# Kernel tuning notes

Measured on AMD Instinct MI355X. Metric: run time of the kernel, lower is better.

Reference implementation:

```python
import jax, jax.numpy as jnp
import numpy as np

B, E, C = 32, 256, 7           # batch, max events, cards per event
D, NA, MP = 256, 8, 9          # d_model, n_actions, max_players
LN_EPS = 1e-5


def setup_inputs() -> dict:
    key = jax.random.key(0)
    ks = jax.random.split(key, 24)

    def tbl(k, shape):  # embedding-table init
        return jax.random.normal(k, shape, jnp.float32) * 0.02

    def lin(k, fan_in, fan_out):  # torch Linear-style init (W stored as (in, out))
        bound = 1.0 / np.sqrt(fan_in)
        k1, k2 = jax.random.split(k)
        W = jax.random.uniform(k1, (fan_in, fan_out), jnp.float32, -bound, bound)
        b = jax.random.uniform(k2, (fan_out,), jnp.float32, -bound, bound)
        return W, b

    W_scalar, b_scalar = lin(ks[10], 2, D)
    W_bet, b_bet = lin(ks[11], MP, D)
    W_action, b_action = lin(ks[12], NA, D)
    W_combine, b_combine = lin(ks[13], D * 7, D)

    return {
        "card_ids": jax.random.randint(ks[0], (B, E, C), 0, 53, jnp.int32),
        "hero_pos": jax.random.randint(ks[1], (B, E), 0, MP, jnp.int32),
        "acting_pos": jax.random.randint(ks[2], (B, E), 0, MP, jnp.int32),
        "num_players": jax.random.randint(ks[3], (B, E), 0, MP + 1, jnp.int32),
        "seq_lengths": jax.random.randint(ks[4], (B,), 1, E + 1, jnp.int32),
        "scalars": jax.random.uniform(ks[5], (B, E, 2), jnp.float32),
        "bets": jax.random.uniform(ks[6], (B, E, MP), jnp.float32),
        "action": jax.random.normal(ks[7], (B, E, NA), jnp.float32),
        "card_table": tbl(ks[14], (53, D)),
        "source_table": tbl(ks[15], (2, D)),
        "hero_table": tbl(ks[16], (MP, D)),
        "acting_table": tbl(ks[17], (MP, D)),
        "nump_table": tbl(ks[18], (MP + 1, D)),
        "W_scalar": W_scalar, "b_scalar": b_scalar,
        "W_bet": W_bet, "b_bet": b_bet,
        "W_action": W_action, "b_action": b_action,
        "W_combine": W_combine, "b_combine": b_combine,
        "ln_gamma": jnp.ones((D,), jnp.float32),
        "ln_beta": jnp.zeros((D,), jnp.float32),
    }


def reference(card_ids, hero_pos, acting_pos, num_players, seq_lengths,
              scalars, bets, action,
              card_table, source_table, hero_table, acting_table, nump_table,
              W_scalar, b_scalar, W_bet, b_bet, W_action, b_action,
              W_combine, b_combine, ln_gamma, ln_beta):
    # gathers
    card_embs = card_table[card_ids]                       # (B,E,7,D)
    source_ids = jnp.array([0, 0, 0, 0, 0, 1, 1], jnp.int32)
    source_embs = source_table[source_ids]                 # (7,D)
    hero_emb = hero_table[hero_pos]                        # (B,E,D)
    acting_emb = acting_table[acting_pos]                  # (B,E,D)
    nump_emb = nump_table[num_players]                     # (B,E,D)
    # small linears
    scalar_emb = scalars @ W_scalar + b_scalar             # (B,E,D)
    bet_emb = bets @ W_bet + b_bet                         # (B,E,D)
    action_emb = action @ W_action + b_action              # (B,E,D)
    # context shared across the 7 cards of an event
    context = jnp.concatenate(
        [hero_emb, acting_emb, nump_emb, scalar_emb, bet_emb, action_emb], axis=-1
    )                                                      # (B,E,6D)
    context = jnp.broadcast_to(context[:, :, None, :], (B, E, C, 6 * D))
    combined = jnp.concatenate([card_embs, context], axis=-1)  # (B,E,7,7D)
    h = combined @ W_combine + b_combine                   # (B,E,7,D)
    # LayerNorm
    mu = jnp.mean(h, axis=-1, keepdims=True)
    var = jnp.mean(jnp.square(h - mu), axis=-1, keepdims=True)
    h = (h - mu) * jax.lax.rsqrt(var + LN_EPS) * ln_gamma + ln_beta
    out = h + source_embs                                  # (B,E,7,D)
    # zero out padded events (original leaves padding as zeros)
    event_mask = (jnp.arange(E)[None, :] < seq_lengths[:, None]).astype(out.dtype)  # (B,E)
    out = out * event_mask[:, :, None, None]
    embeddings = out.reshape(B, E * C, D)
    mask = jnp.repeat(event_mask, C, axis=1)               # (B, E*7)
    return embeddings, mask
```

## Files before the change

kernel.cpp:

```cpp
#include <hip/hip_runtime.h>
#include <hip/hip_bf16.h>
#include <cstddef>

static constexpr int Bdim = 32;
static constexpr int Edim = 256;
static constexpr int Cdim = 7;
static constexpr int Ddim = 256;

__device__ float g_tabs[101 * Ddim];

__global__ __launch_bounds__(256) void precompute_tables(
    const float* __restrict__ card_table,
    const float* __restrict__ hero_table,
    const float* __restrict__ acting_table,
    const float* __restrict__ nump_table,
    const float* __restrict__ W_scalar, const float* __restrict__ b_scalar,
    const float* __restrict__ W_bet,    const float* __restrict__ b_bet,
    const float* __restrict__ W_action, const float* __restrict__ b_action,
    const float* __restrict__ W_combine, const float* __restrict__ b_combine)
{
    __shared__ float src[Ddim];
    const int r = blockIdx.x;
    const int d = threadIdx.x;
    float acc = 0.0f;

    if (r < 100) {
        const float* srcp;
        int off;
        if      (r < 53) { srcp = card_table   + (size_t)r        * Ddim; off = 0;    }
        else if (r < 62) { srcp = hero_table   + (size_t)(r - 53) * Ddim; off = 256;  }
        else if (r < 71) { srcp = acting_table + (size_t)(r - 62) * Ddim; off = 512;  }
        else if (r < 81) { srcp = nump_table   + (size_t)(r - 71) * Ddim; off = 768;  }
        else if (r < 83) { srcp = W_scalar     + (size_t)(r - 81) * Ddim; off = 1024; }
        else if (r < 92) { srcp = W_bet        + (size_t)(r - 83) * Ddim; off = 1280; }
        else             { srcp = W_action     + (size_t)(r - 92) * Ddim; off = 1536; }
        src[d] = srcp[d];
        __syncthreads();
        const float* w = W_combine + (size_t)off * Ddim + d;
        #pragma unroll 4
        for (int k = 0; k < Ddim; ++k)
            acc = fmaf(src[k], w[(size_t)k * Ddim], acc);
    } else {
        const int   offs[3] = {1024, 1280, 1536};
        const float* bias[3] = {b_scalar, b_bet, b_action};
        for (int t = 0; t < 3; ++t) {
            __syncthreads();
            src[d] = bias[t][d];
            __syncthreads();
            const float* w = W_combine + (size_t)offs[t] * Ddim + d;
            #pragma unroll 4
            for (int k = 0; k < Ddim; ++k)
                acc = fmaf(src[k], w[(size_t)k * Ddim], acc);
        }
        acc += b_combine[d];
    }
    g_tabs[(size_t)r * Ddim + d] = acc;
}

__device__ __forceinline__ float4 ld4(const float* p) {
    return *reinterpret_cast<const float4*>(p);
}
__device__ __forceinline__ void add4(float4& a, const float4 b) {
    a.x += b.x; a.y += b.y; a.z += b.z; a.w += b.w;
}
__device__ __forceinline__ void fma4(float4& a, const float s, const float4 b) {
    a.x = fmaf(s, b.x, a.x);
    a.y = fmaf(s, b.y, a.y);
    a.z = fmaf(s, b.z, a.z);
    a.w = fmaf(s, b.w, a.w);
}

__global__ __launch_bounds__(256) void event_embed(
    const int* __restrict__ card_ids,
    const int* __restrict__ hero_pos,
    const int* __restrict__ acting_pos,
    const int* __restrict__ num_players,
    const int* __restrict__ seq_lengths,
    const float* __restrict__ scalars,
    const float* __restrict__ bets,
    const float* __restrict__ action,
    const float* __restrict__ source_table,
    const float* __restrict__ ln_gamma,
    const float* __restrict__ ln_beta,
    float* __restrict__ out_emb,
    float* __restrict__ out_mask)
{
    const int wave = threadIdx.x >> 6;
    const int lane = threadIdx.x & 63;
    const int g = (blockIdx.x << 2) + wave;
    const int b = g >> 8;
    const int e = g & 255;
    const int d0 = lane << 2;

    const float* cardP = g_tabs;
    const float* heroP = cardP + 53 * Ddim;
    const float* actP  = heroP +  9 * Ddim;
    const float* numP  = actP  +  9 * Ddim;
    const float* WsP   = numP  + 10 * Ddim;
    const float* WbP   = WsP   +  2 * Ddim;
    const float* WaP   = WbP   +  9 * Ddim;
    const float* bP    = WaP   +  8 * Ddim;

    const float maskf = (e < seq_lengths[b]) ? 1.0f : 0.0f;

    float4 ctx = ld4(bP + d0);
    add4(ctx, ld4(heroP + (size_t)hero_pos[g]    * Ddim + d0));
    add4(ctx, ld4(actP  + (size_t)acting_pos[g]  * Ddim + d0));
    add4(ctx, ld4(numP  + (size_t)num_players[g] * Ddim + d0));
    fma4(ctx, scalars[(size_t)g * 2 + 0], ld4(WsP + d0));
    fma4(ctx, scalars[(size_t)g * 2 + 1], ld4(WsP + Ddim + d0));
    #pragma unroll
    for (int j = 0; j < 9; ++j)
        fma4(ctx, bets[(size_t)g * 9 + j], ld4(WbP + j * Ddim + d0));
    #pragma unroll
    for (int j = 0; j < 8; ++j)
        fma4(ctx, action[(size_t)g * 8 + j], ld4(WaP + j * Ddim + d0));

    const float4 gam = ld4(ln_gamma + d0);
    const float4 bta = ld4(ln_beta + d0);
    const float4 s0v = ld4(source_table + d0);
    const float4 s1v = ld4(source_table + Ddim + d0);

    #pragma unroll
    for (int c = 0; c < Cdim; ++c) {
        const int cid = card_ids[(size_t)g * Cdim + c];
        float4 h = ld4(cardP + (size_t)cid * Ddim + d0);
        add4(h, ctx);

        float s  = h.x + h.y + h.z + h.w;
        float sq = h.x * h.x + h.y * h.y + h.z * h.z + h.w * h.w;
        #pragma unroll
        for (int off = 32; off > 0; off >>= 1) {
            s  += __shfl_xor(s,  off, 64);
            sq += __shfl_xor(sq, off, 64);
        }
        const float mean = s * (1.0f / 256.0f);
        const float var  = fmaf(-mean, mean, sq * (1.0f / 256.0f));
        const float inv  = rsqrtf(var + 1e-5f);

        const float4 sv = (c < 5) ? s0v : s1v;
        float4 o;
        o.x = (fmaf((h.x - mean) * inv, gam.x, bta.x) + sv.x) * maskf;
        o.y = (fmaf((h.y - mean) * inv, gam.y, bta.y) + sv.y) * maskf;
        o.z = (fmaf((h.z - mean) * inv, gam.z, bta.z) + sv.z) * maskf;
        o.w = (fmaf((h.w - mean) * inv, gam.w, bta.w) + sv.w) * maskf;
        *reinterpret_cast<float4*>(out_emb + ((size_t)g * Cdim + c) * Ddim + d0) = o;
    }

    if (lane < Cdim)
        out_mask[(size_t)g * Cdim + lane] = maskf;
}

extern "C" void kernel_launch(void* const* d_in, const int* in_sizes, int n_in,
                              void* d_out, int out_size, void* d_ws, size_t ws_size,
                              hipStream_t stream)
{
    (void)in_sizes; (void)n_in; (void)d_ws; (void)ws_size; (void)out_size;

    const int*   card_ids    = (const int*)d_in[0];
    const int*   hero_pos    = (const int*)d_in[1];
    const int*   acting_pos  = (const int*)d_in[2];
    const int*   num_players = (const int*)d_in[3];
    const int*   seq_lengths = (const int*)d_in[4];
    const float* scalars     = (const float*)d_in[5];
    const float* bets        = (const float*)d_in[6];
    const float* action      = (const float*)d_in[7];
    const float* card_table  = (const float*)d_in[8];
    const float* source_tab  = (const float*)d_in[9];
    const float* hero_table  = (const float*)d_in[10];
    const float* acting_tab  = (const float*)d_in[11];
    const float* nump_table  = (const float*)d_in[12];
    const float* W_scalar    = (const float*)d_in[13];
    const float* b_scalar    = (const float*)d_in[14];
    const float* W_bet       = (const float*)d_in[15];
    const float* b_bet       = (const float*)d_in[16];
    const float* W_action    = (const float*)d_in[17];
    const float* b_action    = (const float*)d_in[18];
    const float* W_combine   = (const float*)d_in[19];
    const float* b_combine   = (const float*)d_in[20];
    const float* ln_gamma    = (const float*)d_in[21];
    const float* ln_beta     = (const float*)d_in[22];

    float* out_emb  = (float*)d_out;
    float* out_mask = out_emb + (size_t)Bdim * Edim * Cdim * Ddim;

    hipLaunchKernelGGL(precompute_tables, dim3(101), dim3(256), 0, stream,
                       card_table, hero_table, acting_tab, nump_table,
                       W_scalar, b_scalar, W_bet, b_bet, W_action, b_action,
                       W_combine, b_combine);

    const int nEvents = Bdim * Edim;
    hipLaunchKernelGGL(event_embed, dim3(nEvents / 4), dim3(256), 0, stream,
                       card_ids, hero_pos, acting_pos, num_players, seq_lengths,
                       scalars, bets, action, source_tab, ln_gamma, ln_beta,
                       out_emb, out_mask);
}
```

Before: 162.8 us.

## Split table precompute over K chunks and use nontemporal output stores

The table precompute GEMV, which ran on 101 blocks each looping over 256 K values, is split into 808 blocks that each cover a 32-wide K chunk. Partial sums go to workspace and a second small kernel reduces them and adds the combine bias. The main kernel's output writes become nontemporal stores to reduce cache pollution from the large streaming output. This adds one kernel launch and a workspace round-trip, and relies on d_ws being large enough.

```diff
diff --git a/kernel.cpp b/kernel.cpp
--- a/kernel.cpp
+++ b/kernel.cpp
@@ -9,7 +9,7 @@
 
 __device__ float g_tabs[101 * Ddim];
 
-__global__ __launch_bounds__(256) void precompute_tables(
+__global__ __launch_bounds__(256) void precompute_partial(
     const float* __restrict__ card_table,
     const float* __restrict__ hero_table,
     const float* __restrict__ acting_table,
@@ -17,11 +17,12 @@
     const float* __restrict__ W_scalar, const float* __restrict__ b_scalar,
     const float* __restrict__ W_bet,    const float* __restrict__ b_bet,
     const float* __restrict__ W_action, const float* __restrict__ b_action,
-    const float* __restrict__ W_combine, const float* __restrict__ b_combine)
-{
-    __shared__ float src[Ddim];
-    const int r = blockIdx.x;
-    const int d = threadIdx.x;
+    const float* __restrict__ W_combine,
+    float* __restrict__ partials)
+{
+    const int r  = blockIdx.x >> 3;
+    const int kc = blockIdx.x & 7;
+    const int d  = threadIdx.x;
     float acc = 0.0f;
 
     if (r < 100) {
@@ -34,27 +35,36 @@
         else if (r < 83) { srcp = W_scalar     + (size_t)(r - 81) * Ddim; off = 1024; }
         else if (r < 92) { srcp = W_bet        + (size_t)(r - 83) * Ddim; off = 1280; }
         else             { srcp = W_action     + (size_t)(r - 92) * Ddim; off = 1536; }
-        src[d] = srcp[d];
-        __syncthreads();
-        const float* w = W_combine + (size_t)off * Ddim + d;
-        #pragma unroll 4
-        for (int k = 0; k < Ddim; ++k)
-            acc = fmaf(src[k], w[(size_t)k * Ddim], acc);
+        const int k0 = kc << 5;
+        const float* w = W_combine + ((size_t)off + k0) * Ddim + d;
+        #pragma unroll
+        for (int k = 0; k < 32; ++k)
+            acc = fmaf(srcp[k0 + k], w[(size_t)k * Ddim], acc);
     } else {
-        const int   offs[3] = {1024, 1280, 1536};
-        const float* bias[3] = {b_scalar, b_bet, b_action};
-        for (int t = 0; t < 3; ++t) {
-            __syncthreads();
-            src[d] = bias[t][d];
-            __syncthreads();
-            const float* w = W_combine + (size_t)offs[t] * Ddim + d;
-            #pragma unroll 4
-            for (int k = 0; k < Ddim; ++k)
-                acc = fmaf(src[k], w[(size_t)k * Ddim], acc);
+        const int q0 = kc * 96;
+        #pragma unroll
+        for (int q = q0; q < q0 + 96; ++q) {
+            const float s = (q < 256) ? b_scalar[q]
+                          : (q < 512) ? b_bet[q - 256]
+                                      : b_action[q - 512];
+            acc = fmaf(s, W_combine[(size_t)(1024 + q) * Ddim + d], acc);
         }
-        acc += b_combine[d];
     }
-    g_tabs[(size_t)r * Ddim + d] = acc;
+    partials[(size_t)blockIdx.x * Ddim + d] = acc;
+}
+
+__global__ __launch_bounds__(256) void precompute_reduce(
+    const float* __restrict__ partials,
+    const float* __restrict__ b_combine)
+{
+    const int r = blockIdx.x;
+    const int d = threadIdx.x;
+    float v = 0.0f;
+    #pragma unroll
+    for (int kc = 0; kc < 8; ++kc)
+        v += partials[(size_t)(r * 8 + kc) * Ddim + d];
+    if (r == 100) v += b_combine[d];
+    g_tabs[(size_t)r * Ddim + d] = v;
 }
 
 __device__ __forceinline__ float4 ld4(const float* p) {
@@ -69,6 +79,8 @@
     a.z = fmaf(s, b.z, a.z);
     a.w = fmaf(s, b.w, a.w);
 }
+
+typedef float v4f __attribute__((ext_vector_type(4)));
 
 __global__ __launch_bounds__(256) void event_embed(
     const int* __restrict__ card_ids,
@@ -139,12 +151,13 @@
         const float inv  = rsqrtf(var + 1e-5f);
 
         const float4 sv = (c < 5) ? s0v : s1v;
-        float4 o;
+        v4f o;
         o.x = (fmaf((h.x - mean) * inv, gam.x, bta.x) + sv.x) * maskf;
         o.y = (fmaf((h.y - mean) * inv, gam.y, bta.y) + sv.y) * maskf;
         o.z = (fmaf((h.z - mean) * inv, gam.z, bta.z) + sv.z) * maskf;
         o.w = (fmaf((h.w - mean) * inv, gam.w, bta.w) + sv.w) * maskf;
-        *reinterpret_cast<float4*>(out_emb + ((size_t)g * Cdim + c) * Ddim + d0) = o;
+        __builtin_nontemporal_store(
+            o, reinterpret_cast<v4f*>(out_emb + ((size_t)g * Cdim + c) * Ddim + d0));
     }
 
     if (lane < Cdim)
@@ -155,7 +168,7 @@
                               void* d_out, int out_size, void* d_ws, size_t ws_size,
                               hipStream_t stream)
 {
-    (void)in_sizes; (void)n_in; (void)d_ws; (void)ws_size; (void)out_size;
+    (void)in_sizes; (void)n_in; (void)ws_size; (void)out_size;
 
     const int*   card_ids    = (const int*)d_in[0];
     const int*   hero_pos    = (const int*)d_in[1];
@@ -183,11 +196,15 @@
 
     float* out_emb  = (float*)d_out;
     float* out_mask = out_emb + (size_t)Bdim * Edim * Cdim * Ddim;
-
-    hipLaunchKernelGGL(precompute_tables, dim3(101), dim3(256), 0, stream,
+    float* partials = (float*)d_ws;
+
+    hipLaunchKernelGGL(precompute_partial, dim3(101 * 8), dim3(256), 0, stream,
                        card_table, hero_table, acting_tab, nump_table,
                        W_scalar, b_scalar, W_bet, b_bet, W_action, b_action,
-                       W_combine, b_combine);
+                       W_combine, partials);
+
+    hipLaunchKernelGGL(precompute_reduce, dim3(101), dim3(256), 0, stream,
+                       partials, b_combine);
 
     const int nEvents = Bdim * Edim;
     hipLaunchKernelGGL(event_embed, dim3(nEvents / 4), dim3(256), 0, stream,
```

Result: faster. 139.5 us (-14.3%).
